# Optimization experiments

Hardware: AMD Instinct MI355X
Metric: run time of the kernel (lower is better)

The kernel has to match this reference:

```python
import jax, jax.numpy as jnp
import numpy as np
from jax import lax

B, N, C = 2, 4096, 128
HEADS = 4
HD = C // HEADS
EXP = 2  # FFN_expand
EPS = 1e-5


def layernorm(x, w, b):
    mu = jnp.mean(x, axis=-1, keepdims=True)
    var = jnp.mean(jnp.square(x - mu), axis=-1, keepdims=True)
    return (x - mu) * lax.rsqrt(var + EPS) * w + b


def conv2d(x, w, b, pad, groups=1):
    # x: [B, Cin, H, W], w: [Cout, Cin//groups, kh, kw]
    y = lax.conv_general_dilated(
        x, w, window_strides=(1, 1), padding=[(pad, pad), (pad, pad)],
        dimension_numbers=('NCHW', 'OIHW', 'NCHW'), feature_group_count=groups)
    return y + b[None, :, None, None]


def setup_inputs() -> dict:
    key = jax.random.key(0)
    ks = jax.random.split(key, 16)
    C2 = C * EXP
    inp = {
        'x': jax.random.normal(ks[0], (B, N, C), jnp.float32),
        'H': 64,
        'W': 64,
        'ln1_w': jnp.ones((C,), jnp.float32),
        'ln1_b': jnp.zeros((C,), jnp.float32),
        'q_w': jax.random.normal(ks[1], (C, C), jnp.float32) * 0.02,
        'kv_w': jax.random.normal(ks[2], (2 * C, C), jnp.float32) * 0.02,
        'proj_w': jax.random.normal(ks[3], (C, C), jnp.float32) * 0.02,
        'proj_b': jnp.zeros((C,), jnp.float32),
        'ln2_w': jnp.ones((C,), jnp.float32),
        'ln2_b': jnp.zeros((C,), jnp.float32),
        'conv1_w': jax.random.normal(ks[4], (C2, C, 1, 1), jnp.float32) * np.sqrt(2.0 / C2),
        'conv1_b': jnp.zeros((C2,), jnp.float32),
        'conv33_w': jax.random.normal(ks[5], (C2, 1, 3, 3), jnp.float32) * np.sqrt(2.0 / 9),
        'conv33_b': jnp.zeros((C2,), jnp.float32),
        'conv55_w': jax.random.normal(ks[6], (C2, 1, 5, 5), jnp.float32) * np.sqrt(2.0 / 25),
        'conv55_b': jnp.zeros((C2,), jnp.float32),
        'conv4_w': jax.random.normal(ks[7], (C, C, 1, 1), jnp.float32) * np.sqrt(2.0 / C),
        'conv4_b': jnp.zeros((C,), jnp.float32),
    }
    return inp


def reference(x, H, W, ln1_w, ln1_b, q_w, kv_w, proj_w, proj_b,
              ln2_w, ln2_b, conv1_w, conv1_b, conv33_w, conv33_b,
              conv55_w, conv55_b, conv4_w, conv4_b):
    b, n, c = x.shape
    scale = HD ** -0.5

    # ---- Multi-head self-attention (sr_ratio=1) ----
    h = layernorm(x, ln1_w, ln1_b)
    q = jnp.einsum('bnc,oc->bno', h, q_w).reshape(b, n, HEADS, HD).transpose(0, 2, 1, 3)
    kv = jnp.einsum('bnc,oc->bno', h, kv_w).reshape(b, n, 2, HEADS, HD).transpose(2, 0, 3, 1, 4)
    k, v = kv[0], kv[1]
    attn = jnp.einsum('bhqd,bhkd->bhqk', q, k) * scale  # [B, heads, N, N]
    attn = jax.nn.softmax(attn, axis=-1)
    out = jnp.einsum('bhqk,bhkd->bhqd', attn, v).transpose(0, 2, 1, 3).reshape(b, n, c)
    out = jnp.einsum('bnc,oc->bno', out, proj_w) + proj_b
    x = x + out

    # ---- MFFN: conv1 + (dw3x3 + dw5x5) branches, SimpleGate, conv4 ----
    h = layernorm(x, ln2_w, ln2_b)
    hc = h.reshape(b, H, W, c).transpose(0, 3, 1, 2)  # NCHW
    x1 = conv2d(hc, conv1_w, conv1_b, pad=0)
    x33 = conv2d(x1, conv33_w, conv33_b, pad=1, groups=c * EXP)
    x55 = conv2d(x1, conv55_w, conv55_b, pad=2, groups=c * EXP)
    s = x1 + x33 + x55
    a, g = jnp.split(s, 2, axis=1)  # SimpleGate
    gated = a * g
    y = conv2d(gated, conv4_w, conv4_b, pad=0)
    y = y.transpose(0, 2, 3, 1).reshape(b, H * W, c)
    return x + y
```

## Files before the change

kernel.cpp:

```cpp
#include <hip/hip_runtime.h>
#include <hip/hip_bf16.h>
#include <math.h>

#define NB 2
#define NN 4096
#define NC 128
#define NH 4
#define HD 32
#define C2 256
#define HW 64
#define EPS 1e-5f

typedef unsigned short u16;
typedef short bf16x8 __attribute__((ext_vector_type(8)));
typedef unsigned short u16x8 __attribute__((ext_vector_type(8)));
typedef float f32x16 __attribute__((ext_vector_type(16)));

__device__ __forceinline__ u16 f2b(float x) {
    return __bfloat16_as_ushort(__float2bfloat16(x));
}
__device__ __forceinline__ unsigned pack_bf16(float a, float b) {
    return (unsigned)f2b(a) | ((unsigned)f2b(b) << 16);
}
__device__ __forceinline__ f32x16 fzero16() {
    f32x16 z;
    #pragma unroll
    for (int i = 0; i < 16; ++i) z[i] = 0.f;
    return z;
}
union U32x4 { unsigned u[4]; bf16x8 v; };

__device__ __forceinline__ float block_reduce_sum_128(float v, float* sbuf, int tid) {
    #pragma unroll
    for (int off = 32; off > 0; off >>= 1) v += __shfl_xor(v, off, 64);
    __syncthreads();
    if ((tid & 63) == 0) sbuf[tid >> 6] = v;
    __syncthreads();
    return sbuf[0] + sbuf[1];
}

__global__ void k_prep(const float* __restrict__ q_w, const float* __restrict__ kv_w,
                       const float* __restrict__ proj_w, const float* __restrict__ c1_w,
                       const float* __restrict__ c4_w, const float* __restrict__ c33_w,
                       const float* __restrict__ c55_w,
                       u16* wqkv, u16* wproj, u16* wc1, u16* wc4,
                       float* wt33, float* wt55) {
    const int tid = blockIdx.x * blockDim.x + threadIdx.x;
    const int nth = gridDim.x * blockDim.x;
    const float s = 0.17677669529663687f;
    for (int i = tid; i < 128 * 128; i += nth) wqkv[i] = f2b(q_w[i] * s);
    for (int i = tid; i < 256 * 128; i += nth) wqkv[128 * 128 + i] = f2b(kv_w[i]);
    for (int i = tid; i < 128 * 128; i += nth) wproj[i] = f2b(proj_w[i]);
    for (int i = tid; i < 256 * 128; i += nth) wc1[i] = f2b(c1_w[i]);
    for (int i = tid; i < 128 * 128; i += nth) wc4[i] = f2b(c4_w[i]);
    for (int i = tid; i < 9 * 256; i += nth)  { int k = i >> 8, c = i & 255; wt33[i] = c33_w[c * 9 + k]; }
    for (int i = tid; i < 25 * 256; i += nth) { int k = i / 256, c = i % 256; wt55[i] = c55_w[c * 25 + k]; }
}

__global__ __launch_bounds__(128) void k_ln(
    const float* __restrict__ x, const float* __restrict__ w, const float* __restrict__ b,
    u16* __restrict__ h) {
    __shared__ float sred[2];
    const int row = blockIdx.x, tid = threadIdx.x;
    float xv = x[(size_t)row * NC + tid];
    float mean = block_reduce_sum_128(xv, sred, tid) * (1.0f / NC);
    float d = xv - mean;
    float var = block_reduce_sum_128(d * d, sred, tid) * (1.0f / NC);
    float hv = d * rsqrtf(var + EPS) * w[tid] + b[tid];
    h[(size_t)row * NC + tid] = f2b(hv);
}

__device__ __forceinline__ f32x16 gemm_tile_32x32(
    const u16* __restrict__ A, const u16* __restrict__ W, int m0, int n0, int q, int h5) {
    const u16* ap = A + (size_t)(m0 + q) * 128 + h5 * 8;
    const u16* wp = W + (size_t)(n0 + q) * 128 + h5 * 8;
    f32x16 acc = fzero16();
    #pragma unroll
    for (int kk = 0; kk < 8; ++kk) {
        bf16x8 af = *(const bf16x8*)(ap + kk * 16);
        bf16x8 wf = *(const bf16x8*)(wp + kk * 16);
        acc = __builtin_amdgcn_mfma_f32_32x32x16_bf16(af, wf, acc, 0, 0, 0);
    }
    return acc;
}
#define GEMM_PROLOG(NCOLS)                                    \
    const int l = threadIdx.x & 63, wid = threadIdx.x >> 6;   \
    const int q = l & 31, h5 = l >> 5;                        \
    const int m0 = blockIdx.x * 64 + (wid >> 1) * 32;         \
    const int n0 = blockIdx.y * 64 + (wid & 1) * 32;          \
    const int o = n0 + q;                                     \
    (void)o;

__global__ __launch_bounds__(256) void k_gemm_qkv(
    const u16* __restrict__ h1, const u16* __restrict__ wqkv,
    u16* __restrict__ qb, u16* __restrict__ kbuf, u16* __restrict__ vb) {
    GEMM_PROLOG(384)
    f32x16 acc = gemm_tile_32x32(h1, wqkv, m0, n0, q, h5);
    #pragma unroll
    for (int r = 0; r < 16; ++r) {
        const int mr = m0 + (r & 3) + 8 * (r >> 2) + 4 * h5;
        const int b_ = mr >> 12, n = mr & 4095;
        const u16 val = f2b(acc[r]);
        if (o < 128) {
            qb[((size_t)(b_ * 4 + (o >> 5)) * NN + n) * HD + (o & 31)] = val;
        } else if (o < 256) {
            const int o2 = o - 128;
            kbuf[((size_t)(b_ * 4 + (o2 >> 5)) * NN + n) * HD + (o2 & 31)] = val;
        } else {
            vb[(size_t)mr * 128 + (o - 256)] = val;
        }
    }
}

__global__ __launch_bounds__(256) void k_vt(const u16* __restrict__ vb, u16* __restrict__ vtb) {
    __shared__ u16 lds[32][64];
    const int t = threadIdx.x;
    const int bh = blockIdx.y, b_ = bh >> 2, hh = bh & 3;
    const int n0 = blockIdx.x * 64;
    {
        const int i = t >> 2, d0 = (t & 3) * 8;
        u16x8 v = *(const u16x8*)(vb + (size_t)(b_ * NN + n0 + i) * 128 + hh * 32 + d0);
        #pragma unroll
        for (int j = 0; j < 8; ++j) lds[d0 + j][i] = v[j];
    }
    __syncthreads();
    {
        const int d = t >> 3, j0 = (t & 7) * 8;
        u16x8 v;
        #pragma unroll
        for (int u = 0; u < 8; ++u) v[u] = lds[d][j0 + u];
        *(u16x8*)(vtb + ((size_t)bh * 32 + d) * NN + n0 + j0) = v;
    }
}

__global__ __launch_bounds__(256) void k_attn(
    const u16* __restrict__ qb, const u16* __restrict__ kbuf, const u16* __restrict__ vtb,
    u16* __restrict__ ctxb) {
    __shared__ float smx[4][32];
    __shared__ float slv[4][32];
    __shared__ float so[4][64][17];

    const int l = threadIdx.x & 63, w = threadIdx.x >> 6;
    const int q = l & 31, h5 = l >> 5;
    const int bh = blockIdx.y;
    const int qbase = blockIdx.x * 32;

    const u16* qp = qb + ((size_t)bh * NN + qbase + q) * HD + h5 * 8;
    const bf16x8 qf0 = *(const bf16x8*)qp;
    const bf16x8 qf1 = *(const bf16x8*)(qp + 16);

    const int kb0 = w * 1024;
    const u16* kp = kbuf + ((size_t)bh * NN + kb0 + q) * HD + h5 * 8;
    const u16* vp = vtb + ((size_t)bh * 32 + q) * NN + kb0 + h5 * 8;

    float m = -INFINITY, lacc = 0.f;
    f32x16 O = fzero16();

    for (int t = 0; t < 32; ++t) {
        const bf16x8 kf0 = *(const bf16x8*)kp;
        const bf16x8 kf1 = *(const bf16x8*)(kp + 16);
        const bf16x8 vf0 = *(const bf16x8*)vp;
        const bf16x8 vf1 = *(const bf16x8*)(vp + 16);
        kp += 32 * HD;
        vp += 32;

        f32x16 s = fzero16();
        s = __builtin_amdgcn_mfma_f32_32x32x16_bf16(kf0, qf0, s, 0, 0, 0);
        s = __builtin_amdgcn_mfma_f32_32x32x16_bf16(kf1, qf1, s, 0, 0, 0);

        float tm = s[0];
        #pragma unroll
        for (int r = 1; r < 16; ++r) tm = fmaxf(tm, s[r]);
        tm = fmaxf(tm, __shfl_xor(tm, 32));

        if (__any(tm > m + 8.0f)) {
            const float mn = fmaxf(m, tm);
            const float f = __expf(m - mn);
            lacc *= f;
            #pragma unroll
            for (int r = 0; r < 16; ++r) {
                const float fr = __shfl(f, (r & 3) + 8 * (r >> 2) + 4 * h5);
                O[r] *= fr;
            }
            m = mn;
        }

        float p[16];
        float ls = 0.f;
        #pragma unroll
        for (int r = 0; r < 16; ++r) { p[r] = __expf(s[r] - m); ls += p[r]; }
        ls += __shfl_xor(ls, 32);
        lacc += ls;

        unsigned pk[8], ok[8];
        #pragma unroll
        for (int i = 0; i < 8; ++i) pk[i] = pack_bf16(p[2 * i], p[2 * i + 1]);
        #pragma unroll
        for (int i = 0; i < 8; ++i) ok[i] = __shfl_xor(pk[i], 32);

        U32x4 a0, a1;
        if (h5 == 0) {
            a0.u[0] = pk[0]; a0.u[1] = pk[1]; a0.u[2] = ok[0]; a0.u[3] = ok[1];
            a1.u[0] = pk[4]; a1.u[1] = pk[5]; a1.u[2] = ok[4]; a1.u[3] = ok[5];
        } else {
            a0.u[0] = ok[2]; a0.u[1] = ok[3]; a0.u[2] = pk[2]; a0.u[3] = pk[3];
            a1.u[0] = ok[6]; a1.u[1] = ok[7]; a1.u[2] = pk[6]; a1.u[3] = pk[7];
        }
        O = __builtin_amdgcn_mfma_f32_32x32x16_bf16(a0.v, vf0, O, 0, 0, 0);
        O = __builtin_amdgcn_mfma_f32_32x32x16_bf16(a1.v, vf1, O, 0, 0, 0);
    }

    if (l < 32) smx[w][l] = m;
    __syncthreads();
    const float M = fmaxf(fmaxf(smx[0][q], smx[1][q]), fmaxf(smx[2][q], smx[3][q]));
    const float g = __expf(m - M);
    if (l < 32) slv[w][l] = lacc * g;
    #pragma unroll
    for (int r = 0; r < 16; ++r) {
        const float gr = __shfl(g, (r & 3) + 8 * (r >> 2) + 4 * h5);
        so[w][l][r] = O[r] * gr;
    }
    __syncthreads();

    const float Lq = slv[0][q] + slv[1][q] + slv[2][q] + slv[3][q];
    const float linv = 1.0f / Lq;
    const int b_ = bh >> 2, h_ = bh & 3;
    #pragma unroll
    for (int i = 0; i < 4; ++i) {
        const int r = 4 * w + i;
        const float os = so[0][l][r] + so[1][l][r] + so[2][l][r] + so[3][l][r];
        const int qr = (r & 3) + 8 * (r >> 2) + 4 * h5;
        const float fr = __shfl(linv, qr);
        ctxb[((size_t)(b_ * NN + qbase + qr)) * NC + h_ * 32 + q] = f2b(os * fr);
    }
}

__global__ __launch_bounds__(256) void k_gemm_proj(
    const u16* __restrict__ ctxb, const u16* __restrict__ wproj,
    const float* __restrict__ pbias, const float* __restrict__ x, float* __restrict__ x2) {
    GEMM_PROLOG(128)
    f32x16 acc = gemm_tile_32x32(ctxb, wproj, m0, n0, q, h5);
    const float bo = pbias[o];
    #pragma unroll
    for (int r = 0; r < 16; ++r) {
        const int mr = m0 + (r & 3) + 8 * (r >> 2) + 4 * h5;
        x2[(size_t)mr * 128 + o] = acc[r] + bo + x[(size_t)mr * 128 + o];
    }
}

__global__ __launch_bounds__(256) void k_gemm_c1(
    const u16* __restrict__ h2, const u16* __restrict__ wc1,
    const float* __restrict__ bias, float* __restrict__ x1) {
    GEMM_PROLOG(256)
    f32x16 acc = gemm_tile_32x32(h2, wc1, m0, n0, q, h5);
    const float bo = bias[o];
    #pragma unroll
    for (int r = 0; r < 16; ++r) {
        const int mr = m0 + (r & 3) + 8 * (r >> 2) + 4 * h5;
        x1[(size_t)mr * 256 + o] = acc[r] + bo;
    }
}

__global__ __launch_bounds__(128) void k_dwgate(
    const float* __restrict__ x1, const float* __restrict__ wt33, const float* __restrict__ wt55,
    const float* __restrict__ b33, const float* __restrict__ b55, u16* __restrict__ gatedb) {
    const int pb = blockIdx.x, c = threadIdx.x;
    const int b_ = pb >> 12, p = pb & 4095;
    const int py = p >> 6, px = p & 63;
    const float* base = x1 + (size_t)b_ * NN * C2;

    float a5 = 0.f, g5 = 0.f, a3 = 0.f, g3 = 0.f, ca = 0.f, cg = 0.f;
    #pragma unroll
    for (int dy = -2; dy <= 2; ++dy) {
        const int yy = py + dy;
        #pragma unroll
        for (int dx = -2; dx <= 2; ++dx) {
            const int xx = px + dx;
            const bool in = (yy >= 0) && (yy < HW) && (xx >= 0) && (xx < HW);
            const size_t off = (size_t)(yy * HW + xx) * C2;
            const float xa = in ? base[off + c] : 0.f;
            const float xg = in ? base[off + 128 + c] : 0.f;
            const int k5 = (dy + 2) * 5 + (dx + 2);
            a5 += xa * wt55[k5 * 256 + c];
            g5 += xg * wt55[k5 * 256 + 128 + c];
            if (dy >= -1 && dy <= 1 && dx >= -1 && dx <= 1) {
                const int k3 = (dy + 1) * 3 + (dx + 1);
                a3 += xa * wt33[k3 * 256 + c];
                g3 += xg * wt33[k3 * 256 + 128 + c];
            }
            if (dy == 0 && dx == 0) { ca = xa; cg = xg; }
        }
    }
    const float sa = ca + a3 + b33[c] + a5 + b55[c];
    const float sg = cg + g3 + b33[128 + c] + g5 + b55[128 + c];
    gatedb[(size_t)pb * 128 + c] = f2b(sa * sg);
}

__global__ __launch_bounds__(256) void k_gemm_c4(
    const u16* __restrict__ gatedb, const u16* __restrict__ wc4,
    const float* __restrict__ bias, const float* __restrict__ x2, float* __restrict__ out) {
    GEMM_PROLOG(128)
    f32x16 acc = gemm_tile_32x32(gatedb, wc4, m0, n0, q, h5);
    const float bo = bias[o];
    #pragma unroll
    for (int r = 0; r < 16; ++r) {
        const int mr = m0 + (r & 3) + 8 * (r >> 2) + 4 * h5;
        out[(size_t)mr * 128 + o] = acc[r] + bo + x2[(size_t)mr * 128 + o];
    }
}

extern "C" void kernel_launch(void* const* d_in, const int* in_sizes, int n_in,
                              void* d_out, int out_size, void* d_ws, size_t ws_size,
                              hipStream_t stream) {
    const float* x      = (const float*)d_in[0];
    const float* ln1_w  = (const float*)d_in[3];
    const float* ln1_b  = (const float*)d_in[4];
    const float* q_w    = (const float*)d_in[5];
    const float* kv_w   = (const float*)d_in[6];
    const float* proj_w = (const float*)d_in[7];
    const float* proj_b = (const float*)d_in[8];
    const float* ln2_w  = (const float*)d_in[9];
    const float* ln2_b  = (const float*)d_in[10];
    const float* c1_w   = (const float*)d_in[11];
    const float* c1_b   = (const float*)d_in[12];
    const float* c33_w  = (const float*)d_in[13];
    const float* c33_b  = (const float*)d_in[14];
    const float* c55_w  = (const float*)d_in[15];
    const float* c55_b  = (const float*)d_in[16];
    const float* c4_w   = (const float*)d_in[17];
    const float* c4_b   = (const float*)d_in[18];

    char* p = (char*)d_ws;
    u16*   wqkv  = (u16*)p;   p += 384 * 128 * 2;
    u16*   wproj = (u16*)p;   p += 128 * 128 * 2;
    u16*   wc1   = (u16*)p;   p += 256 * 128 * 2;
    u16*   wc4   = (u16*)p;   p += 128 * 128 * 2;
    float* wt33  = (float*)p; p += 9 * 256 * 4;
    float* wt55  = (float*)p; p += 25 * 256 * 4;
    u16*   h1    = (u16*)p;   p += (size_t)8192 * 128 * 2;
    u16*   qb    = (u16*)p;   p += (size_t)8 * 4096 * 32 * 2;
    u16*   kb    = (u16*)p;   p += (size_t)8 * 4096 * 32 * 2;
    u16*   vb    = (u16*)p;   p += (size_t)8192 * 128 * 2;
    u16*   vtb   = (u16*)p;   p += (size_t)8 * 32 * 4096 * 2;
    u16*   ctxb  = (u16*)p;   p += (size_t)8192 * 128 * 2;
    float* x2    = (float*)p; p += (size_t)8192 * 128 * 4;
    u16*   h2    = (u16*)p;   p += (size_t)8192 * 128 * 2;
    float* x1    = (float*)p; p += (size_t)8192 * 256 * 4;
    u16*   gatedb= (u16*)p;   p += (size_t)8192 * 128 * 2;
    float* out   = (float*)d_out;

    k_prep<<<64, 256, 0, stream>>>(q_w, kv_w, proj_w, c1_w, c4_w, c33_w, c55_w,
                                   wqkv, wproj, wc1, wc4, wt33, wt55);
    k_ln<<<NB * NN, 128, 0, stream>>>(x, ln1_w, ln1_b, h1);
    k_gemm_qkv<<<dim3(128, 6), 256, 0, stream>>>(h1, wqkv, qb, kb, vb);
    k_vt<<<dim3(64, 8), 256, 0, stream>>>(vb, vtb);
    k_attn<<<dim3(NN / 32, NB * NH), 256, 0, stream>>>(qb, kb, vtb, ctxb);
    k_gemm_proj<<<dim3(128, 2), 256, 0, stream>>>(ctxb, wproj, proj_b, x, x2);
    k_ln<<<NB * NN, 128, 0, stream>>>(x2, ln2_w, ln2_b, h2);
    k_gemm_c1<<<dim3(128, 4), 256, 0, stream>>>(h2, wc1, c1_b, x1);
    k_dwgate<<<NB * NN, 128, 0, stream>>>(x1, wt33, wt55, c33_b, c55_b, gatedb);
    k_gemm_c4<<<dim3(128, 2), 256, 0, stream>>>(gatedb, wc4, c4_b, x2, out);
}
```

Measured before the change: 209.9 us.

## Fuse proj GEMM with LayerNorm2, use exp2 softmax, prefetch K/V, warp-per-row LN

After: 199.8 us. 4.8% less time.

```diff
diff --git a/kernel.cpp b/kernel.cpp
--- a/kernel.cpp
+++ b/kernel.cpp
@@ -30,13 +30,13 @@
 }
 union U32x4 { unsigned u[4]; bf16x8 v; };
 
-__device__ __forceinline__ float block_reduce_sum_128(float v, float* sbuf, int tid) {
-    #pragma unroll
-    for (int off = 32; off > 0; off >>= 1) v += __shfl_xor(v, off, 64);
-    __syncthreads();
-    if ((tid & 63) == 0) sbuf[tid >> 6] = v;
-    __syncthreads();
-    return sbuf[0] + sbuf[1];
+__device__ __forceinline__ void plswap(unsigned& a, unsigned& b) {
+    asm("v_permlane32_swap_b32 %0, %1" : "+v"(a), "+v"(b));
+}
+__device__ __forceinline__ float xswap(float v, int h5) {
+    float a = v, b = v;
+    asm("v_permlane32_swap_b32 %0, %1" : "+v"(a), "+v"(b));
+    return h5 ? a : b;
 }
 
 __global__ void k_prep(const float* __restrict__ q_w, const float* __restrict__ kv_w,
@@ -47,7 +47,7 @@
                        float* wt33, float* wt55) {
     const int tid = blockIdx.x * blockDim.x + threadIdx.x;
     const int nth = gridDim.x * blockDim.x;
-    const float s = 0.17677669529663687f;
+    const float s = 0.17677669529663687f * 1.4426950408889634f;
     for (int i = tid; i < 128 * 128; i += nth) wqkv[i] = f2b(q_w[i] * s);
     for (int i = tid; i < 256 * 128; i += nth) wqkv[128 * 128 + i] = f2b(kv_w[i]);
     for (int i = tid; i < 128 * 128; i += nth) wproj[i] = f2b(proj_w[i]);
@@ -57,17 +57,26 @@
     for (int i = tid; i < 25 * 256; i += nth) { int k = i / 256, c = i % 256; wt55[i] = c55_w[c * 25 + k]; }
 }
 
-__global__ __launch_bounds__(128) void k_ln(
+__global__ __launch_bounds__(256) void k_ln(
     const float* __restrict__ x, const float* __restrict__ w, const float* __restrict__ b,
     u16* __restrict__ h) {
-    __shared__ float sred[2];
-    const int row = blockIdx.x, tid = threadIdx.x;
-    float xv = x[(size_t)row * NC + tid];
-    float mean = block_reduce_sum_128(xv, sred, tid) * (1.0f / NC);
-    float d = xv - mean;
-    float var = block_reduce_sum_128(d * d, sred, tid) * (1.0f / NC);
-    float hv = d * rsqrtf(var + EPS) * w[tid] + b[tid];
-    h[(size_t)row * NC + tid] = f2b(hv);
+    const int l = threadIdx.x & 63, wid = threadIdx.x >> 6;
+    const int row = blockIdx.x * 4 + wid;
+    const float2 xv = *(const float2*)(x + (size_t)row * NC + l * 2);
+    float sum = xv.x + xv.y, ss = xv.x * xv.x + xv.y * xv.y;
+    #pragma unroll
+    for (int off = 1; off < 64; off <<= 1) {
+        sum += __shfl_xor(sum, off);
+        ss  += __shfl_xor(ss, off);
+    }
+    const float mean = sum * (1.0f / NC);
+    const float var  = ss * (1.0f / NC) - mean * mean;
+    const float rstd = rsqrtf(var + EPS);
+    const float2 wv = *(const float2*)(w + l * 2);
+    const float2 bv = *(const float2*)(b + l * 2);
+    const float h0 = (xv.x - mean) * rstd * wv.x + bv.x;
+    const float h1 = (xv.y - mean) * rstd * wv.y + bv.y;
+    *(unsigned*)(h + (size_t)row * NC + l * 2) = pack_bf16(h0, h1);
 }
 
 __device__ __forceinline__ f32x16 gemm_tile_32x32(
@@ -133,7 +142,7 @@
     }
 }
 
-__global__ __launch_bounds__(256) void k_attn(
+__global__ __launch_bounds__(256, 4) void k_attn(
     const u16* __restrict__ qb, const u16* __restrict__ kbuf, const u16* __restrict__ vtb,
     u16* __restrict__ ctxb) {
     __shared__ float smx[4][32];
@@ -142,8 +151,8 @@
 
     const int l = threadIdx.x & 63, w = threadIdx.x >> 6;
     const int q = l & 31, h5 = l >> 5;
-    const int bh = blockIdx.y;
-    const int qbase = blockIdx.x * 32;
+    const int bh = blockIdx.x;
+    const int qbase = blockIdx.y * 32;
 
     const u16* qp = qb + ((size_t)bh * NN + qbase + q) * HD + h5 * 8;
     const bf16x8 qf0 = *(const bf16x8*)qp;
@@ -156,26 +165,33 @@
     float m = -INFINITY, lacc = 0.f;
     f32x16 O = fzero16();
 
+    bf16x8 kf0 = *(const bf16x8*)kp;
+    bf16x8 kf1 = *(const bf16x8*)(kp + 16);
+    bf16x8 vf0 = *(const bf16x8*)vp;
+    bf16x8 vf1 = *(const bf16x8*)(vp + 16);
+
     for (int t = 0; t < 32; ++t) {
-        const bf16x8 kf0 = *(const bf16x8*)kp;
-        const bf16x8 kf1 = *(const bf16x8*)(kp + 16);
-        const bf16x8 vf0 = *(const bf16x8*)vp;
-        const bf16x8 vf1 = *(const bf16x8*)(vp + 16);
-        kp += 32 * HD;
-        vp += 32;
+        const u16* kpn = kp + ((t < 31) ? 32 * HD : 0);
+        const u16* vpn = vp + ((t < 31) ? 32 : 0);
+        const bf16x8 nk0 = *(const bf16x8*)kpn;
+        const bf16x8 nk1 = *(const bf16x8*)(kpn + 16);
+        const bf16x8 nv0 = *(const bf16x8*)vpn;
+        const bf16x8 nv1 = *(const bf16x8*)(vpn + 16);
 
         f32x16 s = fzero16();
         s = __builtin_amdgcn_mfma_f32_32x32x16_bf16(kf0, qf0, s, 0, 0, 0);
         s = __builtin_amdgcn_mfma_f32_32x32x16_bf16(kf1, qf1, s, 0, 0, 0);
 
-        float tm = s[0];
-        #pragma unroll
-        for (int r = 1; r < 16; ++r) tm = fmaxf(tm, s[r]);
-        tm = fmaxf(tm, __shfl_xor(tm, 32));
+        float t0 = fmaxf(fmaxf(fmaxf(s[0], s[1]), fmaxf(s[2], s[3])),
+                         fmaxf(fmaxf(s[4], s[5]), fmaxf(s[6], s[7])));
+        float t1 = fmaxf(fmaxf(fmaxf(s[8], s[9]), fmaxf(s[10], s[11])),
+                         fmaxf(fmaxf(s[12], s[13]), fmaxf(s[14], s[15])));
+        float tm = fmaxf(t0, t1);
+        tm = fmaxf(tm, xswap(tm, h5));
 
         if (__any(tm > m + 8.0f)) {
             const float mn = fmaxf(m, tm);
-            const float f = __expf(m - mn);
+            const float f = __builtin_amdgcn_exp2f(m - mn);
             lacc *= f;
             #pragma unroll
             for (int r = 0; r < 16; ++r) {
@@ -188,32 +204,33 @@
         float p[16];
         float ls = 0.f;
         #pragma unroll
-        for (int r = 0; r < 16; ++r) { p[r] = __expf(s[r] - m); ls += p[r]; }
-        ls += __shfl_xor(ls, 32);
+        for (int r = 0; r < 16; ++r) { p[r] = __builtin_amdgcn_exp2f(s[r] - m); ls += p[r]; }
+        ls += xswap(ls, h5);
         lacc += ls;
 
-        unsigned pk[8], ok[8];
+        unsigned pk[8];
         #pragma unroll
         for (int i = 0; i < 8; ++i) pk[i] = pack_bf16(p[2 * i], p[2 * i + 1]);
-        #pragma unroll
-        for (int i = 0; i < 8; ++i) ok[i] = __shfl_xor(pk[i], 32);
-
         U32x4 a0, a1;
-        if (h5 == 0) {
-            a0.u[0] = pk[0]; a0.u[1] = pk[1]; a0.u[2] = ok[0]; a0.u[3] = ok[1];
-            a1.u[0] = pk[4]; a1.u[1] = pk[5]; a1.u[2] = ok[4]; a1.u[3] = ok[5];
-        } else {
-            a0.u[0] = ok[2]; a0.u[1] = ok[3]; a0.u[2] = pk[2]; a0.u[3] = pk[3];
-            a1.u[0] = ok[6]; a1.u[1] = ok[7]; a1.u[2] = pk[6]; a1.u[3] = pk[7];
+        {
+            unsigned x0 = pk[0], x2 = pk[2]; plswap(x0, x2);
+            unsigned x1 = pk[1], x3 = pk[3]; plswap(x1, x3);
+            a0.u[0] = x0; a0.u[1] = x1; a0.u[2] = x2; a0.u[3] = x3;
+            unsigned y0 = pk[4], y2 = pk[6]; plswap(y0, y2);
+            unsigned y1 = pk[5], y3 = pk[7]; plswap(y1, y3);
+            a1.u[0] = y0; a1.u[1] = y1; a1.u[2] = y2; a1.u[3] = y3;
         }
         O = __builtin_amdgcn_mfma_f32_32x32x16_bf16(a0.v, vf0, O, 0, 0, 0);
         O = __builtin_amdgcn_mfma_f32_32x32x16_bf16(a1.v, vf1, O, 0, 0, 0);
+
+        kf0 = nk0; kf1 = nk1; vf0 = nv0; vf1 = nv1;
+        kp = kpn; vp = vpn;
     }
 
     if (l < 32) smx[w][l] = m;
     __syncthreads();
     const float M = fmaxf(fmaxf(smx[0][q], smx[1][q]), fmaxf(smx[2][q], smx[3][q]));
-    const float g = __expf(m - M);
+    const float g = __builtin_amdgcn_exp2f(m - M);
     if (l < 32) slv[w][l] = lacc * g;
     #pragma unroll
     for (int r = 0; r < 16; ++r) {
@@ -235,16 +252,53 @@
     }
 }
 
-__global__ __launch_bounds__(256) void k_gemm_proj(
+__global__ __launch_bounds__(256) void k_proj_ln(
     const u16* __restrict__ ctxb, const u16* __restrict__ wproj,
-    const float* __restrict__ pbias, const float* __restrict__ x, float* __restrict__ x2) {
-    GEMM_PROLOG(128)
+    const float* __restrict__ pbias, const float* __restrict__ x,
+    const float* __restrict__ lnw, const float* __restrict__ lnb,
+    float* __restrict__ x2, u16* __restrict__ h2) {
+    __shared__ float sx[32][129];
+    const int l = threadIdx.x & 63, wid = threadIdx.x >> 6;
+    const int q = l & 31, h5 = l >> 5;
+    const int m0 = blockIdx.x * 32;
+    const int n0 = wid * 32;
+    const int o = n0 + q;
+
     f32x16 acc = gemm_tile_32x32(ctxb, wproj, m0, n0, q, h5);
     const float bo = pbias[o];
     #pragma unroll
     for (int r = 0; r < 16; ++r) {
-        const int mr = m0 + (r & 3) + 8 * (r >> 2) + 4 * h5;
-        x2[(size_t)mr * 128 + o] = acc[r] + bo + x[(size_t)mr * 128 + o];
+        const int rr = (r & 3) + 8 * (r >> 2) + 4 * h5;
+        const int mr = m0 + rr;
+        const float xv = acc[r] + bo + x[(size_t)mr * NC + o];
+        x2[(size_t)mr * NC + o] = xv;
+        sx[rr][o] = xv;
+    }
+    __syncthreads();
+
+    const int t = threadIdx.x;
+    const int row = t >> 3, cs = (t & 7) * 16;
+    float vals[16];
+    float sum = 0.f, ss = 0.f;
+    #pragma unroll
+    for (int i = 0; i < 16; ++i) {
+        const float v = sx[row][cs + i];
+        vals[i] = v; sum += v; ss += v * v;
+    }
+    #pragma unroll
+    for (int off = 1; off < 8; off <<= 1) {
+        sum += __shfl_xor(sum, off);
+        ss  += __shfl_xor(ss, off);
+    }
+    const float mean = sum * (1.0f / NC);
+    const float var  = ss * (1.0f / NC) - mean * mean;
+    const float rstd = rsqrtf(var + EPS);
+    const size_t base = (size_t)(m0 + row) * NC + cs;
+    #pragma unroll
+    for (int i = 0; i < 16; i += 2) {
+        const float h0 = (vals[i]     - mean) * rstd * lnw[cs + i]     + lnb[cs + i];
+        const float h1 = (vals[i + 1] - mean) * rstd * lnw[cs + i + 1] + lnb[cs + i + 1];
+        *(unsigned*)(h2 + base + i) = pack_bf16(h0, h1);
     }
 }
 
@@ -351,12 +405,11 @@
 
     k_prep<<<64, 256, 0, stream>>>(q_w, kv_w, proj_w, c1_w, c4_w, c33_w, c55_w,
                                    wqkv, wproj, wc1, wc4, wt33, wt55);
-    k_ln<<<NB * NN, 128, 0, stream>>>(x, ln1_w, ln1_b, h1);
+    k_ln<<<2048, 256, 0, stream>>>(x, ln1_w, ln1_b, h1);
     k_gemm_qkv<<<dim3(128, 6), 256, 0, stream>>>(h1, wqkv, qb, kb, vb);
     k_vt<<<dim3(64, 8), 256, 0, stream>>>(vb, vtb);
-    k_attn<<<dim3(NN / 32, NB * NH), 256, 0, stream>>>(qb, kb, vtb, ctxb);
-    k_gemm_proj<<<dim3(128, 2), 256, 0, stream>>>(ctxb, wproj, proj_b, x, x2);
-    k_ln<<<NB * NN, 128, 0, stream>>>(x2, ln2_w, ln2_b, h2);
+    k_attn<<<dim3(NB * NH, NN / 32), 256, 0, stream>>>(qb, kb, vtb, ctxb);
+    k_proj_ln<<<256, 256, 0, stream>>>(ctxb, wproj, proj_b, x, ln2_w, ln2_b, x2, h2);
     k_gemm_c1<<<dim3(128, 4), 256, 0, stream>>>(h2, wc1, c1_b, x1);
     k_dwgate<<<NB * NN, 128, 0, stream>>>(x1, wt33, wt55, c33_b, c55_b, gatedb);
     k_gemm_c4<<<dim3(128, 2), 256, 0, stream>>>(gatedb, wc4, c4_b, x2, out);
```
